# Optimization experiments

Measured on AMD Instinct MI355X. Metric: run time of the kernel, lower is better.

## Reference

```python
import jax, jax.numpy as jnp
import numpy as np

WS = 5            # window_size
MAXDISP = 192
SUBSCALE = (1, 4)
LEVELS_PER_SCALE = 8


def _grid_sample(img, gx, gy):
    """Bilinear grid_sample, align_corners=True, padding_mode='zeros'.
    img: (B,C,H,W); gx,gy: (B,P) normalized to [-1,1]. Returns (B,C,P)."""
    B, C, H, W = img.shape
    x = (gx + 1.0) * 0.5 * (W - 1)
    y = (gy + 1.0) * 0.5 * (H - 1)
    x0 = jnp.floor(x)
    y0 = jnp.floor(y)
    wx = (x - x0)[:, None, :]
    wy = (y - y0)[:, None, :]
    flat = img.reshape(B, C, H * W)

    def corner(xc, yc):
        valid = (xc >= 0) & (xc <= W - 1) & (yc >= 0) & (yc <= H - 1)
        xi = jnp.clip(xc, 0, W - 1).astype(jnp.int32)
        yi = jnp.clip(yc, 0, H - 1).astype(jnp.int32)
        idx = yi * W + xi                                  # (B,P)
        g = jax.vmap(lambda f, i: f[:, i])(flat, idx)       # (B,C,P)
        return g * valid[:, None, :].astype(img.dtype)

    v00 = corner(x0, y0)
    v01 = corner(x0 + 1.0, y0)
    v10 = corner(x0, y0 + 1.0)
    v11 = corner(x0 + 1.0, y0 + 1.0)
    return (v00 * (1 - wx) * (1 - wy) + v01 * wx * (1 - wy)
            + v10 * (1 - wx) * wy + v11 * wx * wy)


def _forward(left_feats, right_feats, points, img_w, img_h):
    W1 = float(img_w - 1)
    H1 = float(img_h - 1)
    L, _, C, _, _ = left_feats.shape
    B, N, _ = points.shape
    WW = WS * WS

    # Precompute sampling grids once per scale.
    grids = {}
    for scale in SUBSCALE:
        D = MAXDISP // scale
        base = (jnp.arange(WS, dtype=jnp.float32) - WS // 2) * scale  # (WS,)
        xoff = jnp.tile(base, WS)      # x varies fastest within window
        yoff = jnp.repeat(base, WS)
        lx = points[:, :, 0:1] + xoff  # (B,N,WW)
        ly = points[:, :, 1:2] + yoff
        disp = jnp.arange(0, MAXDISP, scale, dtype=jnp.float32)       # (D,)
        rx = lx[:, :, None, :] - disp[None, None, :, None]            # (B,N,D,WW)
        ry = jnp.broadcast_to(ly[:, :, None, :], rx.shape)
        gl = (lx.reshape(B, -1) / W1 * 2.0 - 1.0,
              ly.reshape(B, -1) / H1 * 2.0 - 1.0)
        gr = (rx.reshape(B, -1) / W1 * 2.0 - 1.0,
              ry.reshape(B, -1) / H1 * 2.0 - 1.0)
        grids[scale] = (gl, gr, D)

    costs = []
    for i in range(L):
        scale = SUBSCALE[i // LEVELS_PER_SCALE]
        (glx, gly), (grx, gry), D = grids[scale]
        lf = _grid_sample(left_feats[i], glx, gly).reshape(B, C, N, WW)
        rf = _grid_sample(right_feats[i], grx, gry).reshape(B, C, N, D, WW)
        # mean of |l - r| over channel and window -> (B,N,D)
        cost = jnp.mean(jnp.abs(lf[:, :, :, None, :] - rf), axis=(1, 4))
        cost = 1.0 - jnp.exp(-cost)
        if scale != 1:
            # bilinear upsample D -> MAXDISP along disparity, align_corners=True
            pos = jnp.arange(MAXDISP, dtype=jnp.float32) * (D - 1) / (MAXDISP - 1)
            i0 = jnp.floor(pos).astype(jnp.int32)
            i1 = jnp.minimum(i0 + 1, D - 1)
            w = pos - i0.astype(jnp.float32)
            cost = cost[:, :, i0] * (1.0 - w) + cost[:, :, i1] * w
        costs.append(cost)

    stacked = jnp.stack(costs, axis=-1)                     # (B,N,MAXDISP,L)
    return stacked.reshape(B, N, MAXDISP, len(SUBSCALE), -1).sum(axis=3)


def setup_inputs() -> dict:
    key = jax.random.key(0)
    k1, k2, k3, k4 = jax.random.split(key, 4)
    L, B, C, H, W = 16, 1, 16, 96, 320
    N = 1024
    left_feats = jax.random.normal(k1, (L, B, C, H, W), dtype=jnp.float32)
    right_feats = jax.random.normal(k2, (L, B, C, H, W), dtype=jnp.float32)
    px = jax.random.uniform(k3, (B, N), dtype=jnp.float32) * (W - 1)
    py = jax.random.uniform(k4, (B, N), dtype=jnp.float32) * (H - 1)
    points = jnp.stack([px, py], axis=-1)
    return {"left_feats": left_feats, "right_feats": right_feats,
            "points": points, "img_w": W, "img_h": H}


def reference(left_feats, right_feats, points, img_w, img_h):
    return _forward(left_feats, right_feats, points, img_w, img_h)
```

## Files before the change

kernel.cpp:

```cpp
#include <hip/hip_runtime.h>
#include <hip/hip_fp16.h>

#define MAXD 192
#define NCH  16

#define RFL_I(x) __builtin_amdgcn_readfirstlane(x)
#define RFL_F(x) __int_as_float(__builtin_amdgcn_readfirstlane(__float_as_int(x)))
#define RDLU(v,k) ((unsigned)__builtin_amdgcn_readlane((int)(v), (k)))
#define H2(u) __builtin_bit_cast(__half2, (unsigned)(u))
#define U32(h) __builtin_bit_cast(unsigned, (h))
#define BPERM(idx, v) __int_as_float(__builtin_amdgcn_ds_bpermute((idx), __float_as_int(v)))

struct F2 { float x, y; };
#define LOADF2(base, boff) (*(const F2*)((base) + (boff)))

__global__ __launch_bounds__(256, 8) void pbm_kernel(
    const float* __restrict__ lfeat,
    const float* __restrict__ rfeat,
    const float* __restrict__ points,
    const int* __restrict__ pW, const int* __restrict__ pH,
    float* __restrict__ out)
{
    const int W = RFL_I(*pW), H = RFL_I(*pH);
    const int HW = W * H;
    const int j   = blockIdx.x;
    const int n   = blockIdx.y;
    const int tid = threadIdx.x;
    const int wv  = tid >> 6;
    const int l   = tid & 63;

    const float pxr = points[2 * n];
    const float pyr = points[2 * n + 1];
    const float pxf = floorf(pxr), pyf = floorf(pyr);
    const float fx  = RFL_F(pxr - pxf);
    const float fy  = RFL_F(pyr - pyf);
    const int   x0i = RFL_I((int)pxf);
    const int   y0i = RFL_I((int)pyf);

    __shared__ unsigned svh[4][5][68];
    __shared__ float    val4[48];

    const bool isP0   = (wv == 3);
    const int  s_     = RFL_I(isP0 ? 4 : 1);
    const int  lvl    = RFL_I(isP0 ? j + 8 : j);
    const int  off    = RFL_I(isP0 ? 49 : wv * 64 + 65);
    const int  DC     = RFL_I(isP0 ? 48 : 64);

    const int   cx    = x0i + s_ * (l - off);
    const int   pairB = min(max(cx, 0), W - 2) * 4;
    const float ax0   = (((unsigned)cx       < (unsigned)W) ? 1.0f : 0.0f) * (1.0f - fx);
    const float ax1   = (((unsigned)(cx + 1) < (unsigned)W) ? 1.0f : 0.0f) * fx;
    const float w0    = ((cx >= W - 1) ? 0.f : ax0) + ((cx >= 0) ? 0.f : ax1);
    const float w1    = ((cx >= W - 1) ? ax0 : 0.f) + ((cx >= 0) ? ax1 : 0.f);

    const int   dcx  = x0i + (64 + (l & 3)) - off;
    const float dax0 = (((unsigned)dcx       < (unsigned)W) ? 1.0f : 0.0f) * (1.0f - fx);
    const float dax1 = (((unsigned)(dcx + 1) < (unsigned)W) ? 1.0f : 0.0f) * fx;
    const float w0d  = ((dcx >= W - 1) ? 0.f : dax0) + ((dcx >= 0) ? 0.f : dax1);
    const float w1d  = ((dcx >= W - 1) ? dax0 : 0.f) + ((dcx >= 0) ? dax1 : 0.f);
    const int   voS  = min(max(y0i + min(l >> 2, 5) - 2, 0), H - 1) * (W * 4)
                     + min(max(dcx, 0), W - 2) * 4;
    const int   dyr  = y0i + min(l >> 2, 4) - 2;
    const float dwy0 = ((unsigned)dyr       < (unsigned)H) ? (1.0f - fy) : 0.0f;
    const float dwy1 = ((unsigned)(dyr + 1) < (unsigned)H) ? fy : 0.0f;

    const int   lq = min(l, 35);
    const int   rd = lq / 6;
    const int   cd = lq - rd * 6;
    int lrow, lcx;
    if (isP0) {
        int ls = min(l, 59);
        int ri = ls / 6, cc = ls - ri * 6;
        lrow = y0i + 4 * ((ri >> 1) - 2) + (ri & 1);
        lcx  = x0i + 4 * (min(cc, 4) - 2);
    } else {
        lrow = y0i + rd - 2;
        lcx  = x0i + cd - 2;
    }
    const int   loS  = min(max(lrow, 0), H - 1) * (W * 4) + min(max(lcx, 0), W - 2) * 4;
    const float gx0  = (((unsigned)lcx       < (unsigned)W) ? 1.0f : 0.0f) * (1.0f - fx);
    const float gx1  = (((unsigned)(lcx + 1) < (unsigned)W) ? 1.0f : 0.0f) * fx;
    const float lv0  = ((lcx >= W - 1) ? 0.f : gx0) + ((lcx >= 0) ? 0.f : gx1);
    const float lv1  = ((lcx >= W - 1) ? gx0 : 0.f) + ((lcx >= 0) ? gx1 : 0.f);
    const int   ib0  = isP0 ? (12 * rd + cd) * 4 : (l * 4);
    const int   ib1  = isP0 ? ((12 * rd + cd) * 4 + 24) : ((l + 6) * 4);
    const int   lyd  = y0i + s_ * (rd - 2);
    const float lwy0 = ((unsigned)lyd       < (unsigned)H) ? (1.0f - fy) : 0.0f;
    const float lwy1 = ((unsigned)(lyd + 1) < (unsigned)H) ? fy : 0.0f;

    const char* RbC = (const char*)(rfeat + (size_t)(lvl * NCH) * HW);
    const char* LbC = (const char*)(lfeat + (size_t)(lvl * NCH) * HW);

    float acc = 0.0f;
#pragma unroll 1
    for (int c = 0; c < NCH; c += 2) {
        const char* RpC0 = RbC + (size_t)c * HW * 4;
        const char* RpC1 = RpC0 + (size_t)HW * 4;
        const char* LpC0 = LbC + (size_t)c * HW * 4;
        const char* LpC1 = LpC0 + (size_t)HW * 4;

        F2 e0 = LOADF2(RpC0, voS);
        F2 e1 = LOADF2(RpC1, voS);
        F2 p0 = LOADF2(LpC0, loS);
        F2 p1 = LOADF2(LpC1, loS);

        if (!isP0) {
            int rbp = min(max(y0i - 2, 0), H - 1) * (W * 4);
            F2 a0 = LOADF2(RpC0 + rbp, pairB);
            F2 a1 = LOADF2(RpC1 + rbp, pairB);
            float h0p = fmaf(w0, a0.x, w1 * a0.y);
            float h1p = fmaf(w0, a1.x, w1 * a1.y);
#pragma unroll 2
            for (int yy = 0; yy < 5; ++yy) {
                int   yrc = y0i + yy - 1;
                int   rbc = min(max(yrc, 0), H - 1) * (W * 4);
                F2 c0 = LOADF2(RpC0 + rbc, pairB);
                F2 c1 = LOADF2(RpC1 + rbc, pairB);
                float h0c = fmaf(w0, c0.x, w1 * c0.y);
                float h1c = fmaf(w0, c1.x, w1 * c1.y);
                int   yr  = y0i + yy - 2;
                float wy0 = ((unsigned)yr  < (unsigned)H) ? (1.0f - fy) : 0.0f;
                float wy1 = ((unsigned)yrc < (unsigned)H) ? fy : 0.0f;
                svh[wv][yy][l] = U32(__floats2half2_rn(fmaf(wy0, h0p, wy1 * h0c),
                                                       fmaf(wy0, h1p, wy1 * h1c)));
                h0p = h0c; h1p = h1c;
            }
            {
                float g0 = fmaf(w0d, e0.x, w1d * e0.y);
                float g1 = fmaf(w0d, e1.x, w1d * e1.y);
                float g0n = BPERM((l + 4) * 4, g0);
                float g1n = BPERM((l + 4) * 4, g1);
                if (l < 20)
                    svh[wv][l >> 2][64 + (l & 3)] =
                        U32(__floats2half2_rn(fmaf(dwy0, g0, dwy1 * g0n),
                                              fmaf(dwy0, g1, dwy1 * g1n)));
            }
        } else if (l < 52) {
#pragma unroll 2
            for (int yy = 0; yy < 5; ++yy) {
                int   yr   = y0i + 4 * (yy - 2);
                int   rbB0 = min(max(yr, 0), H - 1) * (W * 4);
                int   rbB1 = min(max(yr + 1, 0), H - 1) * (W * 4);
                float wy0  = ((unsigned)yr       < (unsigned)H) ? (1.0f - fy) : 0.0f;
                float wy1  = ((unsigned)(yr + 1) < (unsigned)H) ? fy : 0.0f;
                F2 a0 = LOADF2(RpC0 + rbB0, pairB);
                F2 b0 = LOADF2(RpC0 + rbB1, pairB);
                F2 a1 = LOADF2(RpC1 + rbB0, pairB);
                F2 b1 = LOADF2(RpC1 + rbB1, pairB);
                float h00 = fmaf(w0, a0.x, w1 * a0.y);
                float h01 = fmaf(w0, b0.x, w1 * b0.y);
                float h10 = fmaf(w0, a1.x, w1 * a1.y);
                float h11 = fmaf(w0, b1.x, w1 * b1.y);
                svh[wv][yy][l] = U32(__floats2half2_rn(fmaf(wy0, h00, wy1 * h01),
                                                       fmaf(wy0, h10, wy1 * h11)));
            }
        }

        unsigned lpk;
        {
            float h0 = fmaf(lv0, p0.x, lv1 * p0.y);
            float h1 = fmaf(lv0, p1.x, lv1 * p1.y);
            float a0 = BPERM(ib0, h0), b0 = BPERM(ib1, h0);
            float a1 = BPERM(ib0, h1), b1 = BPERM(ib1, h1);
            lpk = U32(__floats2half2_rn(fmaf(lwy0, a0, lwy1 * b0),
                                        fmaf(lwy0, a1, lwy1 * b1)));
        }

        if (l < DC) {
            __half2 aE = __floats2half2_rn(0.f, 0.f);
            __half2 aO = __floats2half2_rn(0.f, 0.f);
#define TAPROW(YY) {                                                        \
            const unsigned* rp = &svh[wv][YY][DC - 1 - l];                  \
            unsigned q0 = rp[0], q1 = rp[1], q2 = rp[2], q3 = rp[3], q4 = rp[4];\
            unsigned s0 = RDLU(lpk, (YY)*6+0);                              \
            unsigned s1 = RDLU(lpk, (YY)*6+1);                              \
            unsigned s2 = RDLU(lpk, (YY)*6+2);                              \
            unsigned s3 = RDLU(lpk, (YY)*6+3);                              \
            unsigned s4 = RDLU(lpk, (YY)*6+4);                              \
            aE = __hadd2(aE, __habs2(__hsub2(H2(s0), H2(q0))));             \
            aO = __hadd2(aO, __habs2(__hsub2(H2(s1), H2(q1))));             \
            aE = __hadd2(aE, __habs2(__hsub2(H2(s2), H2(q2))));             \
            aO = __hadd2(aO, __habs2(__hsub2(H2(s3), H2(q3))));             \
            aE = __hadd2(aE, __habs2(__hsub2(H2(s4), H2(q4)))); }
            TAPROW(0)
            TAPROW(1)
            TAPROW(2)
            TAPROW(3)
            TAPROW(4)
#undef TAPROW
            __half2 at = __hadd2(aE, aO);
            acc += __half2float(__low2half(at)) + __half2float(__high2half(at));
        }
    }

    if (isP0 && l < 48)
        val4[l] = 1.0f - expf(-acc * (1.0f / 400.0f));

    __syncthreads();

    if (tid < MAXD) {
        float v1  = 1.0f - expf(-acc * (1.0f / 400.0f));
        float pos = (float)tid * (47.0f / 191.0f);
        float i0f = floorf(pos);
        int   i0  = (int)i0f;
        float w   = pos - i0f;
        int   i1  = min(i0 + 1, 47);
        float up  = val4[i0] + w * (val4[i1] - val4[i0]);
        out[((size_t)n * MAXD + tid) * 8 + j] = v1 + up;
    }
}

extern "C" void kernel_launch(void* const* d_in, const int* in_sizes, int n_in,
                              void* d_out, int out_size, void* d_ws, size_t ws_size,
                              hipStream_t stream) {
    const float* lf  = (const float*)d_in[0];
    const float* rf  = (const float*)d_in[1];
    const float* pts = (const float*)d_in[2];
    const int*   pW  = (const int*)d_in[3];
    const int*   pH  = (const int*)d_in[4];
    float* out = (float*)d_out;

    const int N = in_sizes[2] / 2;
    pbm_kernel<<<dim3(8, N), 256, 0, stream>>>(lf, rf, pts, pW, pH, out);
}
```

Measured before the change: 145.0 us.

## Batch two channel-pair iterations per LDS tap pass using double-buffered packed slots

The shared window buffer becomes a two-slot (8-byte) array, and even and odd channel-pair iterations write alternate slots. The SAD tap loop now runs only on odd iterations, reading both slots with 8-byte LDS loads and accumulating two channel pairs at once. The left-pixel packed value from the even iteration is kept in a register. This halves the number of tap passes and LDS read instructions at the cost of double the LDS footprint, more registers, and some fp16 accumulation reordering. Correctness relies on the existing per-wave ordering of LDS writes and reads with no block barrier.

```diff
diff --git a/kernel.cpp b/kernel.cpp
--- a/kernel.cpp
+++ b/kernel.cpp
@@ -12,6 +12,7 @@
 #define BPERM(idx, v) __int_as_float(__builtin_amdgcn_ds_bpermute((idx), __float_as_int(v)))
 
 struct F2 { float x, y; };
+struct __align__(8) U2 { unsigned x, y; };
 #define LOADF2(base, boff) (*(const F2*)((base) + (boff)))
 
 __global__ __launch_bounds__(256, 8) void pbm_kernel(
@@ -37,8 +38,8 @@
     const int   x0i = RFL_I((int)pxf);
     const int   y0i = RFL_I((int)pyf);
 
-    __shared__ unsigned svh[4][5][68];
-    __shared__ float    val4[48];
+    __shared__ U2    svh[4][5][68];
+    __shared__ float val4[48];
 
     const bool isP0   = (wv == 3);
     const int  s_     = RFL_I(isP0 ? 4 : 1);
@@ -92,8 +93,10 @@
     const char* LbC = (const char*)(lfeat + (size_t)(lvl * NCH) * HW);
 
     float acc = 0.0f;
+    unsigned lpkPrev = 0;
 #pragma unroll 1
     for (int c = 0; c < NCH; c += 2) {
+        const int ph = (c >> 1) & 1;
         const char* RpC0 = RbC + (size_t)c * HW * 4;
         const char* RpC1 = RpC0 + (size_t)HW * 4;
         const char* LpC0 = LbC + (size_t)c * HW * 4;
@@ -121,8 +124,9 @@
                 int   yr  = y0i + yy - 2;
                 float wy0 = ((unsigned)yr  < (unsigned)H) ? (1.0f - fy) : 0.0f;
                 float wy1 = ((unsigned)yrc < (unsigned)H) ? fy : 0.0f;
-                svh[wv][yy][l] = U32(__floats2half2_rn(fmaf(wy0, h0p, wy1 * h0c),
-                                                       fmaf(wy0, h1p, wy1 * h1c)));
+                ((unsigned*)&svh[wv][yy][l])[ph] =
+                    U32(__floats2half2_rn(fmaf(wy0, h0p, wy1 * h0c),
+                                          fmaf(wy0, h1p, wy1 * h1c)));
                 h0p = h0c; h1p = h1c;
             }
             {
@@ -131,7 +135,7 @@
                 float g0n = BPERM((l + 4) * 4, g0);
                 float g1n = BPERM((l + 4) * 4, g1);
                 if (l < 20)
-                    svh[wv][l >> 2][64 + (l & 3)] =
+                    ((unsigned*)&svh[wv][l >> 2][64 + (l & 3)])[ph] =
                         U32(__floats2half2_rn(fmaf(dwy0, g0, dwy1 * g0n),
                                               fmaf(dwy0, g1, dwy1 * g1n)));
             }
@@ -151,8 +155,9 @@
                 float h01 = fmaf(w0, b0.x, w1 * b0.y);
                 float h10 = fmaf(w0, a1.x, w1 * a1.y);
                 float h11 = fmaf(w0, b1.x, w1 * b1.y);
-                svh[wv][yy][l] = U32(__floats2half2_rn(fmaf(wy0, h00, wy1 * h01),
-                                                       fmaf(wy0, h10, wy1 * h11)));
+                ((unsigned*)&svh[wv][yy][l])[ph] =
+                    U32(__floats2half2_rn(fmaf(wy0, h00, wy1 * h01),
+                                          fmaf(wy0, h10, wy1 * h11)));
             }
         }
 
@@ -166,29 +171,39 @@
                                         fmaf(lwy0, a1, lwy1 * b1)));
         }
 
-        if (l < DC) {
+        if (ph == 0) {
+            lpkPrev = lpk;
+        } else if (l < DC) {
+            const unsigned lpkA = lpkPrev, lpkB = lpk;
             __half2 aE = __floats2half2_rn(0.f, 0.f);
             __half2 aO = __floats2half2_rn(0.f, 0.f);
+            __half2 bE = __floats2half2_rn(0.f, 0.f);
+            __half2 bO = __floats2half2_rn(0.f, 0.f);
 #define TAPROW(YY) {                                                        \
-            const unsigned* rp = &svh[wv][YY][DC - 1 - l];                  \
-            unsigned q0 = rp[0], q1 = rp[1], q2 = rp[2], q3 = rp[3], q4 = rp[4];\
-            unsigned s0 = RDLU(lpk, (YY)*6+0);                              \
-            unsigned s1 = RDLU(lpk, (YY)*6+1);                              \
-            unsigned s2 = RDLU(lpk, (YY)*6+2);                              \
-            unsigned s3 = RDLU(lpk, (YY)*6+3);                              \
-            unsigned s4 = RDLU(lpk, (YY)*6+4);                              \
-            aE = __hadd2(aE, __habs2(__hsub2(H2(s0), H2(q0))));             \
-            aO = __hadd2(aO, __habs2(__hsub2(H2(s1), H2(q1))));             \
-            aE = __hadd2(aE, __habs2(__hsub2(H2(s2), H2(q2))));             \
-            aO = __hadd2(aO, __habs2(__hsub2(H2(s3), H2(q3))));             \
-            aE = __hadd2(aE, __habs2(__hsub2(H2(s4), H2(q4)))); }
+            const U2* rp = &svh[wv][YY][DC - 1 - l];                        \
+            U2 q0 = rp[0], q1 = rp[1], q2 = rp[2], q3 = rp[3], q4 = rp[4];  \
+            unsigned sA0 = RDLU(lpkA, (YY)*6+0), sB0 = RDLU(lpkB, (YY)*6+0);\
+            unsigned sA1 = RDLU(lpkA, (YY)*6+1), sB1 = RDLU(lpkB, (YY)*6+1);\
+            unsigned sA2 = RDLU(lpkA, (YY)*6+2), sB2 = RDLU(lpkB, (YY)*6+2);\
+            unsigned sA3 = RDLU(lpkA, (YY)*6+3), sB3 = RDLU(lpkB, (YY)*6+3);\
+            unsigned sA4 = RDLU(lpkA, (YY)*6+4), sB4 = RDLU(lpkB, (YY)*6+4);\
+            aE = __hadd2(aE, __habs2(__hsub2(H2(sA0), H2(q0.x))));          \
+            bE = __hadd2(bE, __habs2(__hsub2(H2(sB0), H2(q0.y))));          \
+            aO = __hadd2(aO, __habs2(__hsub2(H2(sA1), H2(q1.x))));          \
+            bO = __hadd2(bO, __habs2(__hsub2(H2(sB1), H2(q1.y))));          \
+            aE = __hadd2(aE, __habs2(__hsub2(H2(sA2), H2(q2.x))));          \
+            bE = __hadd2(bE, __habs2(__hsub2(H2(sB2), H2(q2.y))));          \
+            aO = __hadd2(aO, __habs2(__hsub2(H2(sA3), H2(q3.x))));          \
+            bO = __hadd2(bO, __habs2(__hsub2(H2(sB3), H2(q3.y))));          \
+            aE = __hadd2(aE, __habs2(__hsub2(H2(sA4), H2(q4.x))));          \
+            bE = __hadd2(bE, __habs2(__hsub2(H2(sB4), H2(q4.y)))); }
             TAPROW(0)
             TAPROW(1)
             TAPROW(2)
             TAPROW(3)
             TAPROW(4)
 #undef TAPROW
-            __half2 at = __hadd2(aE, aO);
+            __half2 at = __hadd2(__hadd2(aE, aO), __hadd2(bE, bO));
             acc += __half2float(__low2half(at)) + __half2float(__high2half(at));
         }
     }
```

Measured after the change: 146.7 us. No clear change (+1.1%).
